# Performance work log

Measured on AMD Instinct MI355X. Metric: run time of the kernel, lower is better.

The kernel has to match this reference:

```python
import jax, jax.numpy as jnp
import numpy as np

VAR_FLOOR = 0.002
BS, A, IN, H, L, NNH, ATT, NACT = 1024, 32, 96, 64, 16, 64, 32, 16


def _lin(x, w, b):
    return x @ w.T + b


def _lrelu(x):
    return jax.nn.leaky_relu(x, 0.01)


def setup_inputs() -> dict:
    key = jax.random.key(0)
    ks = jax.random.split(key, 24)
    def w(k, o, i):
        return jax.random.normal(k, (o, i), jnp.float32) / np.float32(np.sqrt(i))
    def b(k, o):
        return jax.random.normal(k, (o,), jnp.float32) * 0.01
    N = BS * A
    return {
        "inputs": jax.random.normal(ks[0], (N, IN), jnp.float32),
        "hidden_state": jax.random.normal(ks[1], (N, H), jnp.float32),
        "eps": jax.random.normal(ks[2], (N, A * L), jnp.float32),
        "fc1_w": w(ks[3], H, IN), "fc1_b": b(ks[4], H),
        "gru_wih": w(ks[5], 3 * H, H), "gru_whh": w(ks[6], 3 * H, H),
        "gru_bih": b(ks[7], 3 * H), "gru_bhh": b(ks[8], 3 * H),
        "fc2_w": w(ks[9], NACT, H), "fc2_b": b(ks[10], NACT),
        "emb_w1": w(ks[11], NNH, H), "emb_b1": b(ks[12], NNH),
        "bn_g": jnp.ones((NNH,), jnp.float32), "bn_b": jnp.zeros((NNH,), jnp.float32),
        "emb_w2": w(ks[13], A * L * 2, NNH), "emb_b2": b(ks[14], A * L * 2),
        "msg_w1": w(ks[15], NNH, H + L), "msg_b1": b(ks[16], NNH),
        "msg_w2": w(ks[17], NACT, NNH), "msg_b2": b(ks[18], NACT),
        "wq_w": w(ks[19], ATT, H), "wq_b": b(ks[20], ATT),
        "wk_w": w(ks[21], ATT, L), "wk_b": b(ks[22], ATT),
        "bs": BS, "t": 0,
    }


def reference(inputs, hidden_state, eps, fc1_w, fc1_b, gru_wih, gru_whh, gru_bih,
              gru_bhh, fc2_w, fc2_b, emb_w1, emb_b1, bn_g, bn_b, emb_w2, emb_b2,
              msg_w1, msg_b1, msg_w2, msg_b2, wq_w, wq_b, wk_w, wk_b, bs, t):
    Hd = fc1_w.shape[0]
    x = jax.nn.relu(_lin(inputs, fc1_w, fc1_b))
    h_in = hidden_state.reshape(-1, Hd)
    # GRUCell
    gi = _lin(x, gru_wih, gru_bih)
    gh = _lin(h_in, gru_whh, gru_bhh)
    ir, iz, inn = jnp.split(gi, 3, axis=-1)
    hr, hz, hn = jnp.split(gh, 3, axis=-1)
    r = jax.nn.sigmoid(ir + hr)
    z = jax.nn.sigmoid(iz + hz)
    n = jnp.tanh(inn + r * hn)
    h = (1.0 - z) * n + z * h_in
    q = _lin(h, fc2_w, fc2_b)
    # embed_net: Linear -> BatchNorm(train) -> LeakyReLU -> Linear
    z1 = _lin(h, emb_w1, emb_b1)
    z1 = bn_g * (z1 - z1.mean(0)) / jnp.sqrt(z1.var(0) + 1e-5) + bn_b
    lat_par = _lin(_lrelu(z1), emb_w2, emb_b2)
    D = lat_par.shape[-1] // 2
    Ld = wk_w.shape[1]
    Ag = D // Ld
    mu = lat_par[:, :D]
    var = jnp.clip(jnp.exp(lat_par[:, D:]), VAR_FLOOR, None)
    latent = (mu + jnp.sqrt(var) * eps).reshape(bs, Ag, Ag, Ld)  # [b,i,j,L]
    # msg_net on (h of receiver j, latent[b,i,j])
    h3 = h.reshape(bs, Ag, Hd)
    h_rep = jnp.broadcast_to(h3[:, None, :, :], (bs, Ag, Ag, Hd))  # [b,i,j]=h[b,j]
    msg_in = jnp.concatenate([h_rep, latent], axis=-1)
    msg = _lin(_lrelu(_lin(msg_in, msg_w1, msg_b1)), msg_w2, msg_b2)  # (b,A,A,n_act)
    # attention gating
    att = wq_w.shape[0]
    query = _lin(h, wq_w, wq_b).reshape(bs, Ag, att) / np.float32(np.sqrt(att))
    key_ = _lin(latent, wk_w, wk_b)  # (b,A,A,att)
    alpha = jnp.einsum('bia,bija->bij', query, key_)
    alpha = jnp.where(jnp.eye(Ag, dtype=bool)[None], -1e9, alpha)
    alpha = jax.nn.softmax(alpha, axis=-1)
    agg = jnp.einsum('bij,bijn->bjn', alpha, msg)  # sum gated msgs over sender i
    return_q = q + agg.reshape(bs * Ag, -1)
    return (return_q, h)
```

## Files before the change

kernel.cpp:

```cpp
#include <hip/hip_runtime.h>
#include <math.h>

namespace {

constexpr int NROW = 32768;
constexpr int HDIM = 64;
constexpr int DH   = 512;

typedef __attribute__((ext_vector_type(8))) short bf16x8;
typedef __attribute__((ext_vector_type(4))) float f32x4;
typedef __attribute__((ext_vector_type(4))) unsigned uint4e;
typedef __attribute__((ext_vector_type(2))) unsigned uint2e;

__device__ __forceinline__ float sigmoidf_(float x) { return 1.f / (1.f + __expf(-x)); }
__device__ __forceinline__ float lrelu_(float x) { return x > 0.f ? x : 0.01f * x; }
__device__ __forceinline__ unsigned pkbf(float a, float b) {
  unsigned ua = __float_as_uint(a) + 0x8000u;
  unsigned ub = __float_as_uint(b) + 0x8000u;
  return __builtin_amdgcn_perm(ub, ua, 0x07060302);
}

__global__ __launch_bounds__(512, 1) void k_fgru(
    const float* __restrict__ in,
    const float* __restrict__ hprev,
    const float* __restrict__ fc1w, const float* __restrict__ fc1b,
    const float* __restrict__ wih, const float* __restrict__ whh,
    const float* __restrict__ bih, const float* __restrict__ bhh,
    float* __restrict__ hT, float* __restrict__ hout) {
  __shared__ char smem[73728];
  const int t = threadIdx.x;
  const int n0 = blockIdx.x * 128;
  short*    xS = (short*)smem;
  unsigned* gU = (unsigned*)(smem + 18432);
  float*    trF = (float*)(smem + 18432);

  const float2* wih2 = (const float2*)wih;
  const float2* whh2 = (const float2*)whh;
  {
    float2 wv[12];
#pragma unroll
    for (int i = 0; i < 12; ++i) {
      int idx = t + 512 * i;
      int row = idx >> 5, kp = idx & 31;
      wv[i] = wih2[row * 32 + kp];
    }
#pragma unroll
    for (int i = 0; i < 12; ++i) {
      int idx = t + 512 * i;
      int row = idx >> 5, kp = idx & 31;
      int gate = row >> 6, cl = row & 63;
      gU[(gate * 64 + cl) * 36 + kp] = pkbf(wv[i].x, wv[i].y);
    }
#pragma unroll
    for (int i = 0; i < 12; ++i) {
      int idx = t + 512 * i;
      int row = idx >> 5, kp = idx & 31;
      wv[i] = whh2[row * 32 + kp];
    }
#pragma unroll
    for (int i = 0; i < 12; ++i) {
      int idx = t + 512 * i;
      int row = idx >> 5, kp = idx & 31;
      int gate = row >> 6, cl = row & 63;
      gU[((gate + 3) * 64 + cl) * 36 + kp] = pkbf(wv[i].x, wv[i].y);
    }
  }

  const int w = t >> 6, l = t & 63;
  const int m = l & 15, g = l >> 4;
  const int rowA = n0 + w * 16 + m;

  bf16x8 af[3];
#pragma unroll
  for (int ks = 0; ks < 3; ++ks) {
    const float4* p = (const float4*)(in + (size_t)rowA * 96 + ks * 32 + g * 8);
    float4 a = p[0], b = p[1];
    union { unsigned u[4]; bf16x8 h; } tw;
    tw.u[0] = pkbf(a.x, a.y); tw.u[1] = pkbf(a.z, a.w);
    tw.u[2] = pkbf(b.x, b.y); tw.u[3] = pkbf(b.z, b.w);
    af[ks] = tw.h;
  }
  {
    f32x4 accx[4];
#pragma unroll
    for (int ct = 0; ct < 4; ++ct) accx[ct] = (f32x4){0.f, 0.f, 0.f, 0.f};
#pragma unroll
    for (int ct = 0; ct < 4; ++ct)
#pragma unroll
      for (int ks = 0; ks < 3; ++ks) {
        const float4* p = (const float4*)(fc1w + (ct * 16 + m) * 96 + ks * 32 + g * 8);
        float4 a = p[0], b = p[1];
        union { unsigned u[4]; bf16x8 h; } tw;
        tw.u[0] = pkbf(a.x, a.y); tw.u[1] = pkbf(a.z, a.w);
        tw.u[2] = pkbf(b.x, b.y); tw.u[3] = pkbf(b.z, b.w);
        accx[ct] = __builtin_amdgcn_mfma_f32_16x16x32_bf16(af[ks], tw.h, accx[ct], 0, 0, 0);
      }
#pragma unroll
    for (int ct = 0; ct < 4; ++ct) {
      int c = ct * 16 + m;
      float bc = fc1b[c];
#pragma unroll
      for (int reg = 0; reg < 4; ++reg) {
        int nl = w * 16 + g * 4 + reg;
        float v = fmaxf(accx[ct][reg] + bc, 0.f);
        xS[nl * 72 + c] = (short)((__float_as_uint(v) + 0x8000u) >> 16);
      }
    }
  }
  __syncthreads();

  bf16x8 ax[2], ah[2];
#pragma unroll
  for (int ks = 0; ks < 2; ++ks) {
    ax[ks] = *(const bf16x8*)(xS + (w * 16 + m) * 72 + ks * 32 + g * 8);
    const float4* p = (const float4*)(hprev + (size_t)rowA * 64 + ks * 32 + g * 8);
    float4 a = p[0], b = p[1];
    union { unsigned u[4]; bf16x8 h; } tw;
    tw.u[0] = pkbf(a.x, a.y); tw.u[1] = pkbf(a.z, a.w);
    tw.u[2] = pkbf(b.x, b.y); tw.u[3] = pkbf(b.z, b.w);
    ah[ks] = tw.h;
  }
  const short* gS = (const short*)gU;
  float hc[4][4];
#pragma unroll 1
  for (int ct = 0; ct < 4; ++ct) {
    f32x4 a_ir = (f32x4){0.f,0.f,0.f,0.f}, a_iz = (f32x4){0.f,0.f,0.f,0.f},
          a_in = (f32x4){0.f,0.f,0.f,0.f}, a_hr = (f32x4){0.f,0.f,0.f,0.f},
          a_hz = (f32x4){0.f,0.f,0.f,0.f}, a_hn = (f32x4){0.f,0.f,0.f,0.f};
    int crow = ct * 16 + m;
#pragma unroll
    for (int ks = 0; ks < 2; ++ks) {
      bf16x8 b0 = *(const bf16x8*)(gS + (0 * 64 + crow) * 72 + ks * 32 + g * 8);
      bf16x8 b1 = *(const bf16x8*)(gS + (1 * 64 + crow) * 72 + ks * 32 + g * 8);
      bf16x8 b2 = *(const bf16x8*)(gS + (2 * 64 + crow) * 72 + ks * 32 + g * 8);
      bf16x8 b3 = *(const bf16x8*)(gS + (3 * 64 + crow) * 72 + ks * 32 + g * 8);
      bf16x8 b4 = *(const bf16x8*)(gS + (4 * 64 + crow) * 72 + ks * 32 + g * 8);
      bf16x8 b5 = *(const bf16x8*)(gS + (5 * 64 + crow) * 72 + ks * 32 + g * 8);
      a_ir = __builtin_amdgcn_mfma_f32_16x16x32_bf16(ax[ks], b0, a_ir, 0, 0, 0);
      a_iz = __builtin_amdgcn_mfma_f32_16x16x32_bf16(ax[ks], b1, a_iz, 0, 0, 0);
      a_in = __builtin_amdgcn_mfma_f32_16x16x32_bf16(ax[ks], b2, a_in, 0, 0, 0);
      a_hr = __builtin_amdgcn_mfma_f32_16x16x32_bf16(ah[ks], b3, a_hr, 0, 0, 0);
      a_hz = __builtin_amdgcn_mfma_f32_16x16x32_bf16(ah[ks], b4, a_hz, 0, 0, 0);
      a_hn = __builtin_amdgcn_mfma_f32_16x16x32_bf16(ah[ks], b5, a_hn, 0, 0, 0);
    }
    float bir = bih[crow], biz = bih[64 + crow], bin = bih[128 + crow];
    float bhr = bhh[crow], bhz = bhh[64 + crow], bhn = bhh[128 + crow];
#pragma unroll
    for (int reg = 0; reg < 4; ++reg) {
      int nl = w * 16 + g * 4 + reg;
      float hv = hprev[(size_t)(n0 + nl) * 64 + crow];
      float r  = sigmoidf_(a_ir[reg] + bir + a_hr[reg] + bhr);
      float z  = sigmoidf_(a_iz[reg] + biz + a_hz[reg] + bhz);
      float nn = tanhf(a_in[reg] + bin + r * (a_hn[reg] + bhn));
      hc[ct][reg] = (1.f - z) * nn + z * hv;
    }
  }
  __syncthreads();
#pragma unroll
  for (int ct = 0; ct < 4; ++ct)
#pragma unroll
    for (int reg = 0; reg < 4; ++reg)
      trF[(ct * 16 + m) * 133 + w * 16 + g * 4 + reg] = hc[ct][reg];
  __syncthreads();
#pragma unroll
  for (int i = 0; i < 16; ++i) {
    int idx = t + 512 * i;
    int nl = idx & 127, cl = idx >> 7;
    hT[(size_t)cl * NROW + n0 + nl] = trF[cl * 133 + nl];
  }
#pragma unroll
  for (int i = 0; i < 16; ++i) {
    int idx = t + 512 * i;
    int c = idx & 63, nl = idx >> 6;
    hout[(size_t)(n0 + nl) * 64 + c] = trF[c * 133 + nl];
  }
}

__global__ __launch_bounds__(256) void k_heads(const float* __restrict__ hT,
    const float* __restrict__ fc2w, const float* __restrict__ fc2b,
    const float* __restrict__ wqw, const float* __restrict__ wkw,
    const float* __restrict__ ew1, const float* __restrict__ eb1,
    float* __restrict__ qT, float* __restrict__ qkT, float* __restrict__ z1T,
    float* __restrict__ part) {
  __shared__ char smem[36864];
  const int t = threadIdx.x;
  const int n0 = blockIdx.x * 128;
  unsigned* hU = (unsigned*)smem;
  unsigned* wU = (unsigned*)(smem + 18432);
  float* sp1 = (float*)(smem + 18432 + 13824);
  float* sp2 = sp1 + 256;
  const float qs = 0.17677669529663687f;

  {
    float va[16], vb[16];
#pragma unroll
    for (int i = 0; i < 16; ++i) {
      int idx = t + 256 * i;
      int nl = idx & 127, kp = idx >> 7;
      va[i] = hT[(size_t)(2 * kp) * NROW + n0 + nl];
      vb[i] = hT[(size_t)(2 * kp + 1) * NROW + n0 + nl];
    }
#pragma unroll
    for (int i = 0; i < 16; ++i) {
      int idx = t + 256 * i;
      int nl = idx & 127, kp = idx >> 7;
      hU[nl * 36 + kp] = pkbf(va[i], vb[i]);
    }
  }
  {
    float2 wv[10];
#pragma unroll
    for (int i = 0; i < 10; ++i) {
      int idx = t + 256 * i;
      int kp = idx & 31, cl = idx >> 5;
      const float* src = (cl < 16) ? (fc2w + cl * 64) : (ew1 + (cl - 16) * 64);
      wv[i] = *(const float2*)(src + 2 * kp);
    }
#pragma unroll
    for (int i = 0; i < 10; ++i) {
      int idx = t + 256 * i;
      int kp = idx & 31, cl = idx >> 5;
      int dst = (cl < 16) ? cl : (cl + 16);
      wU[dst * 36 + kp] = pkbf(wv[i].x, wv[i].y);
    }
  }
  {
    int kp = t & 31, ll = t >> 5;
#pragma unroll
    for (int h = 0; h < 2; ++h) {
      int row = ll + 8 * h;
      float s0 = 0.f, s1 = 0.f;
#pragma unroll
      for (int a = 0; a < 32; ++a) {
        float wk = wkw[a * 16 + row];
        s0 = fmaf(wk, wqw[a * 64 + 2 * kp], s0);
        s1 = fmaf(wk, wqw[a * 64 + 2 * kp + 1], s1);
      }
      wU[(16 + row) * 36 + kp] = pkbf(s0 * qs, s1 * qs);
    }
  }
  __syncthreads();

  const int w = t >> 6, l = t & 63;
  const int m = l & 15, g = l >> 4;
  const short* sH = (const short*)hU;
  const short* sW = (const short*)wU;

  bf16x8 af[2][2];
#pragma unroll
  for (int mt = 0; mt < 2; ++mt)
#pragma unroll
    for (int ks = 0; ks < 2; ++ks)
      af[mt][ks] = *(const bf16x8*)(sH + (w * 32 + mt * 16 + m) * 72 + ks * 32 + g * 8);

  f32x4 acc[2][6];
#pragma unroll
  for (int mt = 0; mt < 2; ++mt)
#pragma unroll
    for (int ct = 0; ct < 6; ++ct) acc[mt][ct] = (f32x4){0.f, 0.f, 0.f, 0.f};
#pragma unroll
  for (int ct = 0; ct < 6; ++ct)
#pragma unroll
    for (int ks = 0; ks < 2; ++ks) {
      bf16x8 bw = *(const bf16x8*)(sW + (ct * 16 + m) * 72 + ks * 32 + g * 8);
#pragma unroll
      for (int mt = 0; mt < 2; ++mt)
        acc[mt][ct] = __builtin_amdgcn_mfma_f32_16x16x32_bf16(af[mt][ks], bw, acc[mt][ct], 0, 0, 0);
    }

  float s1[4], s2[4];
#pragma unroll
  for (int zt = 0; zt < 4; ++zt) { s1[zt] = 0.f; s2[zt] = 0.f; }
#pragma unroll
  for (int mt = 0; mt < 2; ++mt) {
    int nb = n0 + w * 32 + mt * 16 + g * 4;
    {
      float bc = fc2b[m];
      f32x4 v;
#pragma unroll
      for (int reg = 0; reg < 4; ++reg) v[reg] = acc[mt][0][reg] + bc;
      *(f32x4*)(qT + (size_t)m * NROW + nb) = v;
    }
    *(f32x4*)(qkT + (size_t)m * NROW + nb) = acc[mt][1];
#pragma unroll
    for (int ct = 2; ct < 6; ++ct) {
      int z = (ct - 2) * 16 + m;
      float bc = eb1[z];
      f32x4 v;
#pragma unroll
      for (int reg = 0; reg < 4; ++reg) {
        float zv = acc[mt][ct][reg] + bc;
        v[reg] = zv;
        s1[ct - 2] += zv;
        s2[ct - 2] = fmaf(zv, zv, s2[ct - 2]);
      }
      *(f32x4*)(z1T + (size_t)z * NROW + nb) = v;
    }
  }
#pragma unroll
  for (int zt = 0; zt < 4; ++zt) {
    s1[zt] += __shfl_down(s1[zt], 16, 64);
    s1[zt] += __shfl_down(s1[zt], 32, 64);
    s2[zt] += __shfl_down(s2[zt], 16, 64);
    s2[zt] += __shfl_down(s2[zt], 32, 64);
  }
  if (l < 16) {
#pragma unroll
    for (int zt = 0; zt < 4; ++zt) {
      sp1[w * 64 + zt * 16 + m] = s1[zt];
      sp2[w * 64 + zt * 16 + m] = s2[zt];
    }
  }
  __syncthreads();
  if (t < 64) {
    float a1 = sp1[t] + sp1[64 + t] + sp1[128 + t] + sp1[192 + t];
    float a2 = sp2[t] + sp2[64 + t] + sp2[128 + t] + sp2[192 + t];
    part[(size_t)blockIdx.x * 128 + t] = a1;
    part[(size_t)blockIdx.x * 128 + 64 + t] = a2;
  }
}

__global__ void k_bnstat(const float* __restrict__ part,
    const float* __restrict__ bng, const float* __restrict__ bnb,
    float* __restrict__ stat) {
  int c = threadIdx.x;
  float s1 = 0.f, s2 = 0.f;
  for (int b = 0; b < 256; ++b) {
    s1 += part[(size_t)b * 128 + c];
    s2 += part[(size_t)b * 128 + 64 + c];
  }
  float mean = s1 * (1.f / NROW);
  float var = s2 * (1.f / NROW) - mean * mean;
  float rstd = rsqrtf(var + 1e-5f);
  float sc = bng[c] * rstd;
  stat[c] = sc;
  stat[64 + c] = bnb[c] - mean * sc;
}

__global__ __launch_bounds__(256) void k_emb_gemm(const float* __restrict__ z1T,
    const float* __restrict__ stat,
    const float* __restrict__ ew2, const float* __restrict__ eb2,
    const float* __restrict__ eps,
    unsigned* __restrict__ latB16g) {
  __shared__ char smem[36864];
  const int t = threadIdx.x;
  const int nb = blockIdx.x >> 3;
  const int cb = blockIdx.x & 7;
  const int n0 = nb * 128;
  const int c0 = cb * 64;

  unsigned* aU = (unsigned*)smem;
  unsigned* bmU = (unsigned*)(smem + 18432);
  unsigned* blU = (unsigned*)(smem + 27648);

  const int w = t >> 6, l = t & 63;
  const int m = l & 15, g = l >> 4;

  {
    float za[16], zb[16];
#pragma unroll
    for (int i = 0; i < 16; ++i) {
      int idx = t + 256 * i;
      int nl = idx & 127, kp = idx >> 7;
      za[i] = z1T[(size_t)(2 * kp) * NROW + n0 + nl];
      zb[i] = z1T[(size_t)(2 * kp + 1) * NROW + n0 + nl];
    }
#pragma unroll
    for (int i = 0; i < 16; ++i) {
      int idx = t + 256 * i;
      int nl = idx & 127, kp = idx >> 7;
      float v0 = lrelu_(fmaf(stat[2 * kp], za[i], stat[64 + 2 * kp]));
      float v1 = lrelu_(fmaf(stat[2 * kp + 1], zb[i], stat[64 + 2 * kp + 1]));
      aU[nl * 36 + kp] = pkbf(v0, v1);
    }
  }
  {
    const float2* ew2_2 = (const float2*)ew2;
    float2 wm[8], wl[8];
#pragma unroll
    for (int i = 0; i < 8; ++i) {
      int idx = t + 256 * i;
      int kp = idx & 31, cl = idx >> 5;
      wm[i] = ew2_2[(size_t)(c0 + cl) * 32 + kp];
      wl[i] = ew2_2[(size_t)(512 + c0 + cl) * 32 + kp];
    }
#pragma unroll
    for (int i = 0; i < 8; ++i) {
      int idx = t + 256 * i;
      int kp = idx & 31, cl = idx >> 5;
      bmU[cl * 36 + kp] = pkbf(wm[i].x, wm[i].y);
      blU[cl * 36 + kp] = pkbf(wl[i].x, wl[i].y);
    }
  }
  __syncthreads();

  float epsR[4][2][4];
#pragma unroll
  for (int ct = 0; ct < 4; ++ct)
#pragma unroll
    for (int mt = 0; mt < 2; ++mt)
#pragma unroll
      for (int reg = 0; reg < 4; ++reg)
        epsR[ct][mt][reg] =
            eps[(size_t)(n0 + w * 32 + mt * 16 + g * 4 + reg) * 512 + c0 + ct * 16 + m];

  const short* sA = (const short*)smem;
  const short* sBm = (const short*)(smem + 18432);
  const short* sBl = (const short*)(smem + 27648);

  f32x4 accm[2][4], accl[2][4];
#pragma unroll
  for (int mt = 0; mt < 2; ++mt)
#pragma unroll
    for (int ct = 0; ct < 4; ++ct) {
      accm[mt][ct] = (f32x4){0.f, 0.f, 0.f, 0.f};
      accl[mt][ct] = (f32x4){0.f, 0.f, 0.f, 0.f};
    }
  bf16x8 af[2][2];
#pragma unroll
  for (int mt = 0; mt < 2; ++mt)
#pragma unroll
    for (int ks = 0; ks < 2; ++ks)
      af[mt][ks] = *(const bf16x8*)(sA + (w * 32 + mt * 16 + m) * 72 + ks * 32 + g * 8);
#pragma unroll
  for (int ct = 0; ct < 4; ++ct) {
#pragma unroll
    for (int ks = 0; ks < 2; ++ks) {
      bf16x8 bm = *(const bf16x8*)(sBm + (ct * 16 + m) * 72 + ks * 32 + g * 8);
      bf16x8 bl = *(const bf16x8*)(sBl + (ct * 16 + m) * 72 + ks * 32 + g * 8);
#pragma unroll
      for (int mt = 0; mt < 2; ++mt) {
        accm[mt][ct] = __builtin_amdgcn_mfma_f32_16x16x32_bf16(af[mt][ks], bm, accm[mt][ct], 0, 0, 0);
        accl[mt][ct] = __builtin_amdgcn_mfma_f32_16x16x32_bf16(af[mt][ks], bl, accl[mt][ct], 0, 0, 0);
      }
    }
  }

  const float stdfloor = 0.04472135955f;
  float lat[2][4][4];
#pragma unroll
  for (int ct = 0; ct < 4; ++ct) {
    int cl = ct * 16 + m;
    float ebm = eb2[c0 + cl], ebl = eb2[DH + c0 + cl];
#pragma unroll
    for (int mt = 0; mt < 2; ++mt)
#pragma unroll
      for (int reg = 0; reg < 4; ++reg) {
        float mu = accm[mt][ct][reg] + ebm;
        float lv = accl[mt][ct][reg] + ebl;
        float sd = fmaxf(__expf(0.5f * lv), stdfloor);
        lat[mt][ct][reg] = fmaf(sd, epsR[ct][mt][reg], mu);
      }
  }
  __syncthreads();
  float* outF = (float*)smem;
#pragma unroll
  for (int mt = 0; mt < 2; ++mt)
#pragma unroll
    for (int ct = 0; ct < 4; ++ct)
#pragma unroll
      for (int reg = 0; reg < 4; ++reg)
        outF[(ct * 16 + m) * 133 + w * 32 + mt * 16 + g * 4 + reg] = lat[mt][ct][reg];
  __syncthreads();
#pragma unroll
  for (int i = 0; i < 16; ++i) {
    int idx = t + 256 * i;
    int cp = idx & 31;
    int nl = idx >> 5;
    float v0 = outF[(2 * cp) * 133 + nl];
    float v1 = outF[(2 * cp + 1) * 133 + nl];
    latB16g[(size_t)(n0 + nl) * 256 + cb * 32 + cp] = pkbf(v0, v1);
  }
}

constexpr int LATB_OFF = 0;
constexpr int H3B_OFF  = 40960;
constexpr int W1H_OFF  = 45568;
constexpr int W1L_OFF  = 54784;
constexpr int W2P_OFF  = 57344;
constexpr int ALL_OFF  = 59648;
constexpr int MT_OFF   = 63872;
constexpr int QKL_OFF  = 74112;
__global__ __launch_bounds__(256, 1) void k_msg(
    const unsigned* __restrict__ latB16g, const float* __restrict__ qkT,
    const float* __restrict__ qT, const float* __restrict__ hrow,
    const float* __restrict__ w1, const float* __restrict__ b1,
    const float* __restrict__ w2, const float* __restrict__ b2,
    float* __restrict__ out) {
  __shared__ char smem[76672];
  const int t = threadIdx.x;
  const int b = blockIdx.x;
  const int b32 = b * 32;
  unsigned* latB_dw = (unsigned*)(smem + LATB_OFF);

  {
    const uint4e* g4 = (const uint4e*)latB16g + (size_t)b32 * 64;
#pragma unroll
    for (int half = 0; half < 2; ++half) {
      uint4e v[4];
#pragma unroll
      for (int it = 0; it < 4; ++it) v[it] = g4[t + 256 * (4 * half + it)];
#pragma unroll
      for (int it = 0; it < 4; ++it) {
        int idx = t + 256 * (4 * half + it);
        int i = idx >> 6;
        int rem = idx & 63;
        int j = rem >> 1, hh = rem & 1;
        unsigned* dst = latB_dw + (i * 32 + j) * 10 + hh * 4;
        *(uint2e*)dst = (uint2e){v[it].x, v[it].y};
        *(uint2e*)(dst + 2) = (uint2e){v[it].z, v[it].w};
      }
    }
  }
  {
    float* qkL = (float*)(smem + QKL_OFF);
    int i = t & 31;
    float v0 = qkT[(size_t)((t >> 5)) * NROW + b32 + i];
    float v1 = qkT[(size_t)((t >> 5) + 8) * NROW + b32 + i];
    qkL[i * 20 + (t >> 5)] = v0;
    qkL[i * 20 + (t >> 5) + 8] = v1;
  }
  {
    int cp = t & 31, jj = t >> 5;
    const float2* h2 = (const float2*)hrow;
    float2 hv[4];
#pragma unroll
    for (int it = 0; it < 4; ++it)
      hv[it] = h2[((size_t)(b32 + jj + 8 * it) * 64 + 2 * cp) >> 1];
    unsigned* dst = (unsigned*)(smem + H3B_OFF);
#pragma unroll
    for (int it = 0; it < 4; ++it)
      dst[(jj + 8 * it) * 36 + cp] = pkbf(hv[it].x, hv[it].y);
  }
  {
    int kp = t & 31, cc = t >> 5;
    const float2* w12 = (const float2*)w1;
    float2 wv[8];
#pragma unroll
    for (int it = 0; it < 8; ++it)
      wv[it] = w12[((cc + 8 * it) * 80 + 2 * kp) >> 1];
    unsigned* dst = (unsigned*)(smem + W1H_OFF);
#pragma unroll
    for (int it = 0; it < 8; ++it)
      dst[(cc + 8 * it) * 36 + kp] = pkbf(wv[it].x, wv[it].y);
  }
  {
    int lp = t & 7, cc = t >> 3;
    const float2* w12 = (const float2*)w1;
    float2 wv[2];
#pragma unroll
    for (int it = 0; it < 2; ++it)
      wv[it] = w12[((cc + 32 * it) * 80 + 64 + 2 * lp) >> 1];
    unsigned* dst = (unsigned*)(smem + W1L_OFF);
#pragma unroll
    for (int it = 0; it < 2; ++it)
      dst[(cc + 32 * it) * 10 + lp] = pkbf(wv[it].x, wv[it].y);
  }
  {
    int pp = t & 31, nn = t >> 5;
    const float2* w22 = (const float2*)w2;
    int p = 2 * pp;
    int c = ((p >> 2) & 3) * 16 + (p >> 4) * 4 + (p & 3);
    float2 wv0 = w22[(nn * 64 + c) >> 1];
    float2 wv1 = w22[((nn + 8) * 64 + c) >> 1];
    unsigned* dst = (unsigned*)(smem + W2P_OFF);
    dst[nn * 36 + pp] = pkbf(wv0.x, wv0.y);
    dst[(nn + 8) * 36 + pp] = pkbf(wv1.x, wv1.y);
  }
  __syncthreads();

  {
    const float* qkL = (const float*)(smem + QKL_OFF);
    float* alL = (float*)(smem + ALL_OFF);
#pragma unroll 1
    for (int p = 0; p < 4; ++p) {
      int i = (t >> 5) + 8 * p;
      int j = t & 31;
      const unsigned* lr = latB_dw + (i * 32 + j) * 10;
      float acc = 0.f;
#pragma unroll
      for (int d = 0; d < 8; ++d) {
        unsigned u = lr[d];
        float lo = __uint_as_float(u << 16);
        float hi = __uint_as_float(u & 0xffff0000u);
        acc = fmaf(lo, qkL[i * 20 + 2 * d], acc);
        acc = fmaf(hi, qkL[i * 20 + 2 * d + 1], acc);
      }
      if (j == i) acc = -1e9f;
      float mx = acc;
#pragma unroll
      for (int msk = 16; msk > 0; msk >>= 1) mx = fmaxf(mx, __shfl_xor(mx, msk, 32));
      float e = __expf(acc - mx);
      float s = e;
#pragma unroll
      for (int msk = 16; msk > 0; msk >>= 1) s += __shfl_xor(s, msk, 32);
      alL[i * 33 + j] = e / s;
    }
  }

  const int w = t >> 6, l = t & 63;
  const int n15 = l & 15, q = l >> 4;
  const int jh = w & 1, ibase = (w >> 1) * 16;
  const bool kact = (q < 2);

  f32x4 hp[4];
#pragma unroll
  for (int ct = 0; ct < 4; ++ct) hp[ct] = (f32x4){0.f, 0.f, 0.f, 0.f};
#pragma unroll
  for (int ct = 0; ct < 4; ++ct)
#pragma unroll
    for (int ks = 0; ks < 2; ++ks) {
      bf16x8 aF = *(const bf16x8*)(smem + W1H_OFF + (ct * 16 + n15) * 144 + ks * 64 + q * 16);
      bf16x8 bF = *(const bf16x8*)(smem + H3B_OFF + (jh * 16 + n15) * 144 + ks * 64 + q * 16);
      hp[ct] = __builtin_amdgcn_mfma_f32_16x16x32_bf16(aF, bF, hp[ct], 0, 0, 0);
    }
#pragma unroll
  for (int ct = 0; ct < 4; ++ct)
#pragma unroll
    for (int reg = 0; reg < 4; ++reg)
      hp[ct][reg] += b1[ct * 16 + q * 4 + reg];

  bf16x8 aL[4];
#pragma unroll
  for (int ct = 0; ct < 4; ++ct) {
    union { unsigned u[4]; bf16x8 h; } tmp;
    tmp.u[0] = tmp.u[1] = tmp.u[2] = tmp.u[3] = 0u;
    if (kact) {
      const unsigned* p = (const unsigned*)(smem + W1L_OFF) + (ct * 16 + n15) * 10 + q * 4;
      uint2e d0 = *(const uint2e*)p;
      uint2e d1 = *(const uint2e*)(p + 2);
      tmp.u[0] = d0.x; tmp.u[1] = d0.y; tmp.u[2] = d1.x; tmp.u[3] = d1.y;
    }
    aL[ct] = tmp.h;
  }
  bf16x8 w2F[2];
#pragma unroll
  for (int ks = 0; ks < 2; ++ks)
    w2F[ks] = *(const bf16x8*)(smem + W2P_OFF + n15 * 144 + ks * 64 + q * 16);
  float b2v[4];
#pragma unroll
  for (int reg = 0; reg < 4; ++reg) b2v[reg] = b2[q * 4 + reg];

  __syncthreads();

  float agg[4] = {0.f, 0.f, 0.f, 0.f};
  char* wb = smem + MT_OFF + w * 2560;
  const float* alLf = (const float*)(smem + ALL_OFF);
#pragma unroll 1
  for (int it = 0; it < 16; ++it) {
    int ii = ibase + it;
    int r = ii * 32 + jh * 16 + n15;
    union { unsigned u[4]; bf16x8 h; } latF;
    latF.u[0] = latF.u[1] = latF.u[2] = latF.u[3] = 0u;
    if (kact) {
      const unsigned* p = latB_dw + r * 10 + q * 4;
      uint2e d0 = *(const uint2e*)p;
      uint2e d1 = *(const uint2e*)(p + 2);
      latF.u[0] = d0.x; latF.u[1] = d0.y; latF.u[2] = d1.x; latF.u[3] = d1.y;
    }
    f32x4 acc[4];
#pragma unroll
    for (int ct = 0; ct < 4; ++ct) {
      acc[ct] = (f32x4){0.f, 0.f, 0.f, 0.f};
      acc[ct] = __builtin_amdgcn_mfma_f32_16x16x32_bf16(aL[ct], latF.h, acc[ct], 0, 0, 0);
    }
#pragma unroll
    for (int h = 0; h < 2; ++h) {
      float m0[4], m1[4];
#pragma unroll
      for (int reg = 0; reg < 4; ++reg) {
        float v0 = acc[2 * h][reg] + hp[2 * h][reg];
        float v1 = acc[2 * h + 1][reg] + hp[2 * h + 1][reg];
        m0[reg] = fmaxf(v0, 0.01f * v0);
        m1[reg] = fmaxf(v1, 0.01f * v1);
      }
      uint4e pk4;
      pk4.x = pkbf(m0[0], m0[1]); pk4.y = pkbf(m0[2], m0[3]);
      pk4.z = pkbf(m1[0], m1[1]); pk4.w = pkbf(m1[2], m1[3]);
      int qp = (2 * q + h) & 3;
      *(uint4e*)(wb + (q >> 1) * 1280 + n15 * 80 + qp * 16) = pk4;
    }
    f32x4 msg = (f32x4){0.f, 0.f, 0.f, 0.f};
#pragma unroll
    for (int ks = 0; ks < 2; ++ks) {
      bf16x8 mF = *(const bf16x8*)(wb + ks * 1280 + n15 * 80 + q * 16);
      msg = __builtin_amdgcn_mfma_f32_16x16x32_bf16(w2F[ks], mF, msg, 0, 0, 0);
    }
    float aw = alLf[ii * 33 + jh * 16 + n15];
#pragma unroll
    for (int reg = 0; reg < 4; ++reg)
      agg[reg] = fmaf(aw, msg[reg] + b2v[reg], agg[reg]);
  }
  {
    f32x4 av; av[0] = agg[0]; av[1] = agg[1]; av[2] = agg[2]; av[3] = agg[3];
    *(f32x4*)(wb + n15 * 80 + q * 16) = av;
  }
  __syncthreads();
#pragma unroll
  for (int tt = 0; tt < 2; ++tt) {
    int idx = t + 256 * tt;
    int jg = idx >> 4, nn = idx & 15;
    int jh2 = jg >> 4, jl = jg & 15;
    float a0 = *(const float*)(smem + MT_OFF + jh2 * 2560 + jl * 80 + nn * 4);
    float a1 = *(const float*)(smem + MT_OFF + (jh2 + 2) * 2560 + jl * 80 + nn * 4);
    out[(size_t)b * 512 + idx] = a0 + a1 + qT[(size_t)nn * NROW + b32 + jg];
  }
}

}

extern "C" void kernel_launch(void* const* d_in, const int* in_sizes, int n_in,
                              void* d_out, int out_size, void* d_ws, size_t ws_size,
                              hipStream_t stream) {
  (void)in_sizes; (void)n_in; (void)out_size; (void)ws_size;
  const float* inputs = (const float*)d_in[0];
  const float* hidden = (const float*)d_in[1];
  const float* eps    = (const float*)d_in[2];
  const float* fc1w   = (const float*)d_in[3];
  const float* fc1b   = (const float*)d_in[4];
  const float* wih    = (const float*)d_in[5];
  const float* whh    = (const float*)d_in[6];
  const float* bih    = (const float*)d_in[7];
  const float* bhh    = (const float*)d_in[8];
  const float* fc2w   = (const float*)d_in[9];
  const float* fc2b   = (const float*)d_in[10];
  const float* ew1    = (const float*)d_in[11];
  const float* eb1    = (const float*)d_in[12];
  const float* bng    = (const float*)d_in[13];
  const float* bnb    = (const float*)d_in[14];
  const float* ew2    = (const float*)d_in[15];
  const float* eb2    = (const float*)d_in[16];
  const float* w1     = (const float*)d_in[17];
  const float* b1     = (const float*)d_in[18];
  const float* w2     = (const float*)d_in[19];
  const float* b2     = (const float*)d_in[20];
  const float* wqw    = (const float*)d_in[21];
  const float* wkw    = (const float*)d_in[23];

  float* ws = (float*)d_ws;
  float* hT     = ws;
  float* qT     = ws + 2097152;
  float* qkT    = ws + 2621440;
  float* z1T    = ws + 3670016;
  float* part   = ws + 5767168;
  float* stat   = ws + 5832704;
  unsigned* latB16g = (unsigned*)(ws + 5832832);

  float* out_q = (float*)d_out;
  float* out_h = (float*)d_out + 524288;

  hipLaunchKernelGGL(k_fgru, dim3(256), dim3(512), 0, stream,
                     inputs, hidden, fc1w, fc1b, wih, whh, bih, bhh, hT, out_h);
  hipLaunchKernelGGL(k_heads, dim3(256), dim3(256), 0, stream,
                     hT, fc2w, fc2b, wqw, wkw, ew1, eb1, qT, qkT, z1T, part);
  hipLaunchKernelGGL(k_bnstat, dim3(1), dim3(64), 0, stream, part, bng, bnb, stat);
  hipLaunchKernelGGL(k_emb_gemm, dim3(2048), dim3(256), 0, stream, z1T, stat, ew2, eb2, eps, latB16g);
  hipLaunchKernelGGL(k_msg, dim3(1024), dim3(256), 0, stream,
                     latB16g, qkT, qT, out_h, w1, b1, w2, b2, out_q);
}
```

Measured before the change: 254.6 us.

## Restructure emb GEMM to loop over column blocks with double-buffered weights

```diff
diff --git a/kernel.cpp b/kernel.cpp
--- a/kernel.cpp
+++ b/kernel.cpp
@@ -337,139 +337,154 @@
   stat[64 + c] = bnb[c] - mean * sc;
 }
 
-__global__ __launch_bounds__(256) void k_emb_gemm(const float* __restrict__ z1T,
+__global__ __launch_bounds__(512, 1) void k_emb_gemm(const float* __restrict__ z1T,
     const float* __restrict__ stat,
     const float* __restrict__ ew2, const float* __restrict__ eb2,
     const float* __restrict__ eps,
     unsigned* __restrict__ latB16g) {
-  __shared__ char smem[36864];
+  __shared__ char smem[55296];
   const int t = threadIdx.x;
-  const int nb = blockIdx.x >> 3;
-  const int cb = blockIdx.x & 7;
-  const int n0 = nb * 128;
-  const int c0 = cb * 64;
+  const int n0 = blockIdx.x * 128;
 
   unsigned* aU = (unsigned*)smem;
-  unsigned* bmU = (unsigned*)(smem + 18432);
-  unsigned* blU = (unsigned*)(smem + 27648);
+  unsigned* wB0 = (unsigned*)(smem + 18432);
+  unsigned* wB1 = (unsigned*)(smem + 36864);
 
   const int w = t >> 6, l = t & 63;
   const int m = l & 15, g = l >> 4;
-
-  {
-    float za[16], zb[16];
-#pragma unroll
-    for (int i = 0; i < 16; ++i) {
-      int idx = t + 256 * i;
+  const float2* ew2_2 = (const float2*)ew2;
+  const float stdfloor = 0.04472135955f;
+
+  {
+    float va[8], vb[8];
+#pragma unroll
+    for (int i = 0; i < 8; ++i) {
+      int idx = t + 512 * i;
       int nl = idx & 127, kp = idx >> 7;
-      za[i] = z1T[(size_t)(2 * kp) * NROW + n0 + nl];
-      zb[i] = z1T[(size_t)(2 * kp + 1) * NROW + n0 + nl];
-    }
-#pragma unroll
-    for (int i = 0; i < 16; ++i) {
-      int idx = t + 256 * i;
+      va[i] = z1T[(size_t)(2 * kp) * NROW + n0 + nl];
+      vb[i] = z1T[(size_t)(2 * kp + 1) * NROW + n0 + nl];
+    }
+#pragma unroll
+    for (int i = 0; i < 8; ++i) {
+      int idx = t + 512 * i;
       int nl = idx & 127, kp = idx >> 7;
-      float v0 = lrelu_(fmaf(stat[2 * kp], za[i], stat[64 + 2 * kp]));
-      float v1 = lrelu_(fmaf(stat[2 * kp + 1], zb[i], stat[64 + 2 * kp + 1]));
+      float v0 = lrelu_(fmaf(stat[2 * kp], va[i], stat[64 + 2 * kp]));
+      float v1 = lrelu_(fmaf(stat[2 * kp + 1], vb[i], stat[64 + 2 * kp + 1]));
       aU[nl * 36 + kp] = pkbf(v0, v1);
     }
   }
-  {
-    const float2* ew2_2 = (const float2*)ew2;
-    float2 wm[8], wl[8];
-#pragma unroll
-    for (int i = 0; i < 8; ++i) {
-      int idx = t + 256 * i;
-      int kp = idx & 31, cl = idx >> 5;
-      wm[i] = ew2_2[(size_t)(c0 + cl) * 32 + kp];
-      wl[i] = ew2_2[(size_t)(512 + c0 + cl) * 32 + kp];
-    }
-#pragma unroll
-    for (int i = 0; i < 8; ++i) {
-      int idx = t + 256 * i;
-      int kp = idx & 31, cl = idx >> 5;
-      bmU[cl * 36 + kp] = pkbf(wm[i].x, wm[i].y);
-      blU[cl * 36 + kp] = pkbf(wl[i].x, wl[i].y);
-    }
-  }
-  __syncthreads();
-
-  float epsR[4][2][4];
+
+  float2 wm[4], wl[4];
+#pragma unroll
+  for (int i = 0; i < 4; ++i) {
+    int idx = t + 512 * i;
+    int kp = idx & 31, cl = idx >> 5;
+    wm[i] = ew2_2[(size_t)cl * 32 + kp];
+    wl[i] = ew2_2[(size_t)(512 + cl) * 32 + kp];
+  }
+#pragma unroll
+  for (int i = 0; i < 4; ++i) {
+    int idx = t + 512 * i;
+    int kp = idx & 31, cl = idx >> 5;
+    wB0[cl * 36 + kp] = pkbf(wm[i].x, wm[i].y);
+    wB0[(64 + cl) * 36 + kp] = pkbf(wl[i].x, wl[i].y);
+  }
+#pragma unroll
+  for (int i = 0; i < 4; ++i) {
+    int idx = t + 512 * i;
+    int kp = idx & 31, cl = idx >> 5;
+    wm[i] = ew2_2[(size_t)(64 + cl) * 32 + kp];
+    wl[i] = ew2_2[(size_t)(512 + 64 + cl) * 32 + kp];
+  }
+  float epsC[16];
 #pragma unroll
   for (int ct = 0; ct < 4; ++ct)
 #pragma unroll
-    for (int mt = 0; mt < 2; ++mt)
-#pragma unroll
-      for (int reg = 0; reg < 4; ++reg)
-        epsR[ct][mt][reg] =
-            eps[(size_t)(n0 + w * 32 + mt * 16 + g * 4 + reg) * 512 + c0 + ct * 16 + m];
-
-  const short* sA = (const short*)smem;
-  const short* sBm = (const short*)(smem + 18432);
-  const short* sBl = (const short*)(smem + 27648);
-
-  f32x4 accm[2][4], accl[2][4];
-#pragma unroll
-  for (int mt = 0; mt < 2; ++mt)
+    for (int reg = 0; reg < 4; ++reg)
+      epsC[ct * 4 + reg] =
+          eps[(size_t)(n0 + w * 16 + g * 4 + reg) * 512 + ct * 16 + m];
+  __syncthreads();
+
+  const short* sA = (const short*)aU;
+  bf16x8 af[2];
+#pragma unroll
+  for (int ks = 0; ks < 2; ++ks)
+    af[ks] = *(const bf16x8*)(sA + (w * 16 + m) * 72 + ks * 32 + g * 8);
+
+  const int rowG = n0 + w * 16 + g * 4;
+
+#pragma unroll 1
+  for (int cb = 0; cb < 8; ++cb) {
+    const int c0 = cb * 64;
+    unsigned* wbC = (cb & 1) ? wB1 : wB0;
+    unsigned* wbN = (cb & 1) ? wB0 : wB1;
+
+    if (cb < 7) {
+#pragma unroll
+      for (int i = 0; i < 4; ++i) {
+        int idx = t + 512 * i;
+        int kp = idx & 31, cl = idx >> 5;
+        wbN[cl * 36 + kp] = pkbf(wm[i].x, wm[i].y);
+        wbN[(64 + cl) * 36 + kp] = pkbf(wl[i].x, wl[i].y);
+      }
+    }
+    if (cb < 6) {
+      int c2 = (cb + 2) * 64;
+#pragma unroll
+      for (int i = 0; i < 4; ++i) {
+        int idx = t + 512 * i;
+        int kp = idx & 31, cl = idx >> 5;
+        wm[i] = ew2_2[(size_t)(c2 + cl) * 32 + kp];
+        wl[i] = ew2_2[(size_t)(512 + c2 + cl) * 32 + kp];
+      }
+    }
+    float epsN[16];
+    if (cb < 7) {
+#pragma unroll
+      for (int ct = 0; ct < 4; ++ct)
+#pragma unroll
+        for (int reg = 0; reg < 4; ++reg)
+          epsN[ct * 4 + reg] =
+              eps[(size_t)(rowG + reg) * 512 + c0 + 64 + ct * 16 + m];
+    }
+
+    const short* sW = (const short*)wbC;
+    f32x4 accm[4], accl[4];
 #pragma unroll
     for (int ct = 0; ct < 4; ++ct) {
-      accm[mt][ct] = (f32x4){0.f, 0.f, 0.f, 0.f};
-      accl[mt][ct] = (f32x4){0.f, 0.f, 0.f, 0.f};
-    }
-  bf16x8 af[2][2];
-#pragma unroll
-  for (int mt = 0; mt < 2; ++mt)
-#pragma unroll
-    for (int ks = 0; ks < 2; ++ks)
-      af[mt][ks] = *(const bf16x8*)(sA + (w * 32 + mt * 16 + m) * 72 + ks * 32 + g * 8);
-#pragma unroll
-  for (int ct = 0; ct < 4; ++ct) {
-#pragma unroll
-    for (int ks = 0; ks < 2; ++ks) {
-      bf16x8 bm = *(const bf16x8*)(sBm + (ct * 16 + m) * 72 + ks * 32 + g * 8);
-      bf16x8 bl = *(const bf16x8*)(sBl + (ct * 16 + m) * 72 + ks * 32 + g * 8);
-#pragma unroll
-      for (int mt = 0; mt < 2; ++mt) {
-        accm[mt][ct] = __builtin_amdgcn_mfma_f32_16x16x32_bf16(af[mt][ks], bm, accm[mt][ct], 0, 0, 0);
-        accl[mt][ct] = __builtin_amdgcn_mfma_f32_16x16x32_bf16(af[mt][ks], bl, accl[mt][ct], 0, 0, 0);
-      }
-    }
-  }
-
-  const float stdfloor = 0.04472135955f;
-  float lat[2][4][4];
-#pragma unroll
-  for (int ct = 0; ct < 4; ++ct) {
-    int cl = ct * 16 + m;
-    float ebm = eb2[c0 + cl], ebl = eb2[DH + c0 + cl];
-#pragma unroll
-    for (int mt = 0; mt < 2; ++mt)
+      accm[ct] = (f32x4){0.f, 0.f, 0.f, 0.f};
+      accl[ct] = (f32x4){0.f, 0.f, 0.f, 0.f};
+    }
+#pragma unroll
+    for (int ct = 0; ct < 4; ++ct)
+#pragma unroll
+      for (int ks = 0; ks < 2; ++ks) {
+        bf16x8 bm = *(const bf16x8*)(sW + (ct * 16 + m) * 72 + ks * 32 + g * 8);
+        bf16x8 bl = *(const bf16x8*)(sW + (64 + ct * 16 + m) * 72 + ks * 32 + g * 8);
+        accm[ct] = __builtin_amdgcn_mfma_f32_16x16x32_bf16(af[ks], bm, accm[ct], 0, 0, 0);
+        accl[ct] = __builtin_amdgcn_mfma_f32_16x16x32_bf16(af[ks], bl, accl[ct], 0, 0, 0);
+      }
+
+#pragma unroll
+    for (int ct = 0; ct < 4; ++ct) {
+      int c = c0 + ct * 16 + m;
+      float ebm = eb2[c], ebl = eb2[DH + c];
 #pragma unroll
       for (int reg = 0; reg < 4; ++reg) {
-        float mu = accm[mt][ct][reg] + ebm;
-        float lv = accl[mt][ct][reg] + ebl;
+        float mu = accm[ct][reg] + ebm;
+        float lv = accl[ct][reg] + ebl;
         float sd = fmaxf(__expf(0.5f * lv), stdfloor);
-        lat[mt][ct][reg] = fmaf(sd, epsR[ct][mt][reg], mu);
-      }
-  }
-  __syncthreads();
-  float* outF = (float*)smem;
-#pragma unroll
-  for (int mt = 0; mt < 2; ++mt)
-#pragma unroll
-    for (int ct = 0; ct < 4; ++ct)
-#pragma unroll
-      for (int reg = 0; reg < 4; ++reg)
-        outF[(ct * 16 + m) * 133 + w * 32 + mt * 16 + g * 4 + reg] = lat[mt][ct][reg];
-  __syncthreads();
-#pragma unroll
-  for (int i = 0; i < 16; ++i) {
-    int idx = t + 256 * i;
-    int cp = idx & 31;
-    int nl = idx >> 5;
-    float v0 = outF[(2 * cp) * 133 + nl];
-    float v1 = outF[(2 * cp + 1) * 133 + nl];
-    latB16g[(size_t)(n0 + nl) * 256 + cb * 32 + cp] = pkbf(v0, v1);
+        float lat = fmaf(sd, epsC[ct * 4 + reg], mu);
+        float lat2 = __shfl_xor(lat, 1, 64);
+        if (!(m & 1)) {
+          latB16g[(size_t)(rowG + reg) * 256 + (c0 >> 1) + ct * 8 + (m >> 1)] =
+              pkbf(lat, lat2);
+        }
+      }
+    }
+#pragma unroll
+    for (int i2 = 0; i2 < 16; ++i2) epsC[i2] = epsN[i2];
+    __syncthreads();
   }
 }
 
@@ -754,7 +769,7 @@
   hipLaunchKernelGGL(k_heads, dim3(256), dim3(256), 0, stream,
                      hT, fc2w, fc2b, wqw, wkw, ew1, eb1, qT, qkT, z1T, part);
   hipLaunchKernelGGL(k_bnstat, dim3(1), dim3(64), 0, stream, part, bng, bnb, stat);
-  hipLaunchKernelGGL(k_emb_gemm, dim3(2048), dim3(256), 0, stream, z1T, stat, ew2, eb2, eps, latB16g);
+  hipLaunchKernelGGL(k_emb_gemm, dim3(256), dim3(512), 0, stream, z1T, stat, ew2, eb2, eps, latB16g);
   hipLaunchKernelGGL(k_msg, dim3(1024), dim3(256), 0, stream,
                      latB16g, qkT, qT, out_h, w1, b1, w2, b2, out_q);
 }
```

New measurement: 250.0 us. About the same (-1.8%).
